# Kernel optimization log

Measured on AMD Instinct MI355X. Metric: run time of the kernel, lower is better.

Reference implementation:

```python
import jax, jax.numpy as jnp
import numpy as np

jax.config.update("jax_enable_x64", True)  # hash math uses int64, matching torch promotion

NUM_LEVELS = 16
MIN_RES = 16
MAX_RES = 1024
LOG2_T = 19
T = 2 ** LOG2_T          # hash table size per level
FEATS = 2                # features per level
HASH_INIT_SCALE = 0.001
N = 524288               # number of query points

# 8 cube corners; bit==1 selects ceil coordinate (weight = offset), bit==0 selects floor (weight = 1-offset)
CORNER_BITS = np.array([[(b >> 2) & 1, (b >> 1) & 1, b & 1] for b in range(8)], dtype=np.int64)
PRIMES = np.array([1, 2654435761, 805459861], dtype=np.int64)


def setup_inputs() -> dict:
    key = jax.random.key(0)
    k1, k2 = jax.random.split(key)
    x = jax.random.uniform(k1, (N, 3), dtype=jnp.float32, minval=-1.0, maxval=1.0)
    hash_table = (jax.random.uniform(k2, (T * NUM_LEVELS, FEATS), dtype=jnp.float32) * 2.0 - 1.0) * HASH_INIT_SCALE
    return {"x": x, "hash_table": hash_table}


def reference(x, hash_table):
    # per-level resolutions: floor(min_res * growth^level)
    growth = np.exp((np.log(MAX_RES) - np.log(MIN_RES)) / (NUM_LEVELS - 1))
    scalings = jnp.asarray(np.floor(MIN_RES * growth ** np.arange(NUM_LEVELS)), dtype=jnp.float32)  # [L]
    hash_offset = jnp.arange(NUM_LEVELS, dtype=jnp.int64) * T  # [L]

    x01 = x * 0.5 + 0.5                                # map [-1,1] -> [0,1]
    scaled = x01[..., None, :] * scalings[:, None]     # [N, L, 3]
    sc = jnp.ceil(scaled).astype(jnp.int64)            # [N, L, 3]
    sf = jnp.floor(scaled).astype(jnp.int64)           # [N, L, 3]
    offset = scaled - sf.astype(scaled.dtype)          # [N, L, 3] in [0,1)

    bits = jnp.asarray(CORNER_BITS)                    # [8, 3]
    # corner integer coords: [N, L, 8, 3]
    corners = jnp.where(bits[None, None] == 1, sc[:, :, None, :], sf[:, :, None, :])

    # Instant-NGP spatial hash (int64, matching torch's type promotion)
    p = corners * jnp.asarray(PRIMES)
    h = jnp.bitwise_xor(jnp.bitwise_xor(p[..., 0], p[..., 1]), p[..., 2])
    h = h % T + hash_offset[None, :, None]             # [N, L, 8]

    # trilinear weights: prod over dims of (offset if ceil else 1-offset)
    w = jnp.prod(jnp.where(bits[None, None] == 1, offset[:, :, None, :], 1.0 - offset[:, :, None, :]), axis=-1)  # [N, L, 8]

    feats = hash_table[h]                              # [N, L, 8, F] gather
    enc = jnp.sum(feats * w[..., None], axis=-2)       # [N, L, F]
    return enc.reshape(*enc.shape[:-2], NUM_LEVELS * FEATS)  # [N, L*F]
```

## Files before the change

### kernel.cpp

```cpp
#include <hip/hip_runtime.h>
#include <cmath>

#define TBL_SIZE (1u << 19)
#define TBL_MASK (TBL_SIZE - 1u)
#define PRIME1 2654435761u
#define PRIME2 805459861u
#define NUM_LEVELS 16
#define PPB 32

#define D0g 17
#define D1g 22
#define D2g 28
#define NW0 (D0g*D0g*D0g)
#define NW1 (D1g*D1g*D1g)
#define NW2 (D2g*D2g*D2g)
#define NWTOT (NW0+NW1+NW2)
#define PAD0 (D0g*D0g+D0g+1)
#define PAD1 (D1g*D1g+D1g+1)
#define PAD2 (D2g*D2g+D2g+1)
#define LB0  0
#define LB1  (LB0+NW0+PAD0)
#define LB2  (LB1+NW1+PAD1)
#define LTOT (LB2+NW2+PAD2)
#define LDSB (LTOT*4)

struct Args { float s[NUM_LEVELS]; };

typedef float v2f __attribute__((ext_vector_type(2)));
typedef float v4f __attribute__((ext_vector_type(4)));

template<int CTRL>
__device__ __forceinline__ float dpp_add(float v) {
    int i = __builtin_bit_cast(int, v);
    int j = __builtin_amdgcn_mov_dpp(i, CTRL, 0xF, 0xF, true);
    return v + __builtin_bit_cast(float, j);
}

__device__ __forceinline__ uint32_t f2bf(float f) {
    uint32_t u = __builtin_bit_cast(uint32_t, f);
    return (u + 0x7FFFu + ((u >> 16) & 1u)) >> 16;
}
__device__ __forceinline__ float bflo(uint32_t v) { return __builtin_bit_cast(float, v << 16); }
__device__ __forceinline__ float bfhi(uint32_t v) { return __builtin_bit_cast(float, v & 0xFFFF0000u); }

__global__ __launch_bounds__(256) void prep_kernel(
    const float* __restrict__ table, uint32_t* __restrict__ bfws,
    uint32_t* __restrict__ densews, int ncvt)
{
    int gid = blockIdx.x * 256 + (int)threadIdx.x;
    if (gid < NWTOT) {
        int l, rel, D;
        if (gid < NW0)            { l = 0; rel = gid;             D = D0g; }
        else if (gid < NW0 + NW1) { l = 1; rel = gid - NW0;       D = D1g; }
        else                      { l = 2; rel = gid - NW0 - NW1; D = D2g; }
        int d2 = D * D;
        int xp = rel / d2; int rem = rel - xp * d2;
        int yp = rem / D;  int zp = rem - yp * D;
        uint32_t h = (uint32_t)xp ^ ((uint32_t)yp * PRIME1) ^ ((uint32_t)zp * PRIME2);
        float2 e = reinterpret_cast<const float2*>(table)[((size_t)l << 19) + (h & TBL_MASK)];
        densews[gid] = f2bf(e.x) | (f2bf(e.y) << 16);
    } else {
        int rel = gid - NWTOT;
        if (rel >= ncvt) return;
        float2 e = reinterpret_cast<const float2*>(table)[((size_t)3 << 19) + rel];
        bfws[rel] = f2bf(e.x) | (f2bf(e.y) << 16);
    }
}

__global__ __launch_bounds__(1024) void lds_levels_kernel(
    const float* __restrict__ x, const uint32_t* __restrict__ densews,
    float* __restrict__ out, int npoints,
    float s0, float s1, float s2)
{
    extern __shared__ uint32_t lds[];
    for (int i = (int)threadIdx.x; i < LTOT; i += 1024) lds[i] = 0;
    __syncthreads();
    for (int i = (int)threadIdx.x; i < NW0; i += 1024) lds[LB0 + i] = densews[i];
    for (int i = (int)threadIdx.x; i < NW1; i += 1024) lds[LB1 + i] = densews[NW0 + i];
    for (int i = (int)threadIdx.x; i < NW2; i += 1024) lds[LB2 + i] = densews[NW0 + NW1 + i];
    __syncthreads();

    float acc[6];
    for (int n = blockIdx.x * 1024 + (int)threadIdx.x; n < npoints; n += (int)gridDim.x * 1024) {
        float x0 = x[(size_t)n * 3 + 0] * 0.5f + 0.5f;
        float x1 = x[(size_t)n * 3 + 1] * 0.5f + 0.5f;
        float x2 = x[(size_t)n * 3 + 2] * 0.5f + 0.5f;

#define DO_LEVEL(LI, DCONST, LBASE, SCALE)                                        \
        {                                                                         \
            const int D = DCONST, D2 = DCONST * DCONST;                           \
            float sx = x0 * SCALE, sy = x1 * SCALE, sz = x2 * SCALE;              \
            float fx = floorf(sx), fy = floorf(sy), fz = floorf(sz);              \
            float ox = sx - fx, oy = sy - fy, oz = sz - fz;                       \
            int base = LBASE + ((int)fx * D + (int)fy) * D + (int)fz;             \
            uint32_t v000 = lds[base];            uint32_t v001 = lds[base + 1];  \
            uint32_t v010 = lds[base + D];        uint32_t v011 = lds[base + D + 1]; \
            uint32_t v100 = lds[base + D2];       uint32_t v101 = lds[base + D2 + 1]; \
            uint32_t v110 = lds[base + D2 + D];   uint32_t v111 = lds[base + D2 + D + 1]; \
            float gx0 = 1.f - ox, gy0 = 1.f - oy, gz0 = 1.f - oz;                 \
            float w000 = gx0 * gy0 * gz0, w001 = gx0 * gy0 * oz;                  \
            float w010 = gx0 * oy * gz0,  w011 = gx0 * oy * oz;                   \
            float w100 = ox * gy0 * gz0,  w101 = ox * gy0 * oz;                   \
            float w110 = ox * oy * gz0,   w111 = ox * oy * oz;                    \
            acc[LI*2+0] = bflo(v000)*w000 + bflo(v001)*w001 + bflo(v010)*w010     \
                        + bflo(v011)*w011 + bflo(v100)*w100 + bflo(v101)*w101     \
                        + bflo(v110)*w110 + bflo(v111)*w111;                      \
            acc[LI*2+1] = bfhi(v000)*w000 + bfhi(v001)*w001 + bfhi(v010)*w010     \
                        + bfhi(v011)*w011 + bfhi(v100)*w100 + bfhi(v101)*w101     \
                        + bfhi(v110)*w110 + bfhi(v111)*w111;                      \
        }
        DO_LEVEL(0, D0g, LB0, s0)
        DO_LEVEL(1, D1g, LB1, s1)
        DO_LEVEL(2, D2g, LB2, s2)
#undef DO_LEVEL

        v4f a; a.x = acc[0]; a.y = acc[1]; a.z = acc[2]; a.w = acc[3];
        v2f b; b.x = acc[4]; b.y = acc[5];
        float* o = out + (size_t)n * 32;
        __builtin_nontemporal_store(a, (v4f*)o);
        __builtin_nontemporal_store(b, (v2f*)(o + 4));
    }
}

__global__ __launch_bounds__(256) void HashEncoding_88837103551034_kernel(
    const float* __restrict__ x,
    const float* __restrict__ table,
    const uint32_t* __restrict__ bfws,
    float* __restrict__ out,
    int npoints, int CH, int perXcd, int total, int L0, int NBF,
    Args args)
{
    int b = blockIdx.x; int xcd = b & 7; int sb = b >> 3;
    int g = xcd * perXcd + sb;
    if (g >= total) return;
    int li = g / CH; int level = L0 + li; int chunk = g - li * CH;
    int t = (int)threadIdx.x;
    int corner = t & 7;
    int n = chunk * PPB + (t >> 3);
    if (n >= npoints) return;

    float x0 = x[(size_t)n * 3 + 0] * 0.5f + 0.5f;
    float x1 = x[(size_t)n * 3 + 1] * 0.5f + 0.5f;
    float x2 = x[(size_t)n * 3 + 2] * 0.5f + 0.5f;
    float sl = args.s[level];
    float sx = x0 * sl, sy = x1 * sl, sz = x2 * sl;
    float fx = floorf(sx), fy = floorf(sy), fz = floorf(sz);
    float ox = sx - fx, oy = sy - fy, oz = sz - fz;
    int bx = (corner >> 2) & 1, by = (corner >> 1) & 1, bz = corner & 1;

    uint32_t h = (uint32_t)((int)fx + bx)
               ^ ((uint32_t)((int)fy + by) * PRIME1)
               ^ ((uint32_t)((int)fz + bz) * PRIME2);
    uint32_t idx = h & TBL_MASK;

    float f0, f1;
    if (li < NBF) {
        uint32_t v = bfws[((size_t)li << 19) + idx];
        f0 = bflo(v); f1 = bfhi(v);
    } else {
        float2 f = reinterpret_cast<const float2*>(table)[((size_t)level << 19) + idx];
        f0 = f.x; f1 = f.y;
    }
    float w = (bx ? ox : 1.f - ox) * (by ? oy : 1.f - oy) * (bz ? oz : 1.f - oz);
    float e0 = f0 * w, e1 = f1 * w;
    e0 = dpp_add<0xB1>(e0);  e1 = dpp_add<0xB1>(e1);
    e0 = dpp_add<0x4E>(e0);  e1 = dpp_add<0x4E>(e1);
    e0 = dpp_add<0x141>(e0); e1 = dpp_add<0x141>(e1);
    if (corner == 0) {
        v2f res; res.x = e0; res.y = e1;
        __builtin_nontemporal_store(res, (v2f*)(out + (size_t)n * 32 + level * 2));
    }
}

extern "C" void kernel_launch(void* const* d_in, const int* in_sizes, int n_in,
                              void* d_out, int out_size, void* d_ws, size_t ws_size,
                              hipStream_t stream) {
    const float* x = (const float*)d_in[0];
    const float* table = (const float*)d_in[1];
    float* out = (float*)d_out;
    int npoints = in_sizes[0] / 3;

    Args args;
    double growth = std::exp((std::log(1024.0) - std::log(16.0)) / 15.0);
    for (int l = 0; l < NUM_LEVELS; ++l)
        args.s[l] = (float)std::floor(16.0 * std::pow(growth, (double)l));

    int CH = (npoints + PPB - 1) / PPB;
    uint32_t* ws32 = (uint32_t*)d_ws;

    bool dimsOk = ((int)args.s[0] == 16) && ((int)args.s[1] == 21) && ((int)args.s[2] == 27);
    size_t needA = ((size_t)13 * TBL_SIZE + (size_t)NWTOT) * 4;

    if (dimsOk && ws_size >= needA) {
        uint32_t* wsdense = ws32 + (size_t)13 * TBL_SIZE;
        int ncvt = 13 << 19;
        int ptot = NWTOT + ncvt;
        prep_kernel<<<(ptot + 255) / 256, 256, 0, stream>>>(table, ws32, wsdense, ncvt);

        hipFuncSetAttribute(reinterpret_cast<const void*>(lds_levels_kernel),
                            hipFuncAttributeMaxDynamicSharedMemorySize, LDSB);
        lds_levels_kernel<<<256, 1024, LDSB, stream>>>(
            x, wsdense, out, npoints, args.s[0], args.s[1], args.s[2]);

        int total = 13 * CH;
        int perXcd = (total + 7) / 8;
        HashEncoding_88837103551034_kernel<<<8 * perXcd, 256, 0, stream>>>(
            x, table, ws32, out, npoints, CH, perXcd, total, 3, 13, args);
    } else {
        int total = 16 * CH;
        int perXcd = (total + 7) / 8;
        HashEncoding_88837103551034_kernel<<<8 * perXcd, 256, 0, stream>>>(
            x, table, ws32, out, npoints, CH, perXcd, total, 0, 0, args);
    }
}
```

Before: 251.6 us.

## Serve levels 3 and 4 from x-sliced dense LDS grids instead of hashing

Adds levels 3 and 4 (resolutions 36 and 48) to the dense, collision-free precomputed grids. Since those grids exceed LDS, each is split into x-slabs, and extra blocks of the LDS kernel each load one slab, scan all points, and handle only those whose floor x falls in the slab. This moves two levels' eight-corner gathers from global hash-table reads to LDS reads. In exchange every slab block re-reads x for all points, and the grid grows to 640 blocks while the hashed kernel shrinks to 11 levels.

```diff
diff --git a/kernel.cpp b/kernel.cpp
--- a/kernel.cpp
+++ b/kernel.cpp
@@ -7,14 +7,21 @@
 #define PRIME2 805459861u
 #define NUM_LEVELS 16
 #define PPB 32
+#define NHASH 11
 
 #define D0g 17
 #define D1g 22
 #define D2g 28
+#define D3g 38
+#define D4g 50
 #define NW0 (D0g*D0g*D0g)
 #define NW1 (D1g*D1g*D1g)
 #define NW2 (D2g*D2g*D2g)
-#define NWTOT (NW0+NW1+NW2)
+#define NW3 (D3g*D3g*D3g)
+#define NW4 (D4g*D4g*D4g)
+#define DB3 (NW0+NW1+NW2)
+#define DB4 (DB3+NW3)
+#define NWALL (DB4+NW4)
 #define PAD0 (D0g*D0g+D0g+1)
 #define PAD1 (D1g*D1g+D1g+1)
 #define PAD2 (D2g*D2g+D2g+1)
@@ -48,11 +55,13 @@
     uint32_t* __restrict__ densews, int ncvt)
 {
     int gid = blockIdx.x * 256 + (int)threadIdx.x;
-    if (gid < NWTOT) {
+    if (gid < NWALL) {
         int l, rel, D;
-        if (gid < NW0)            { l = 0; rel = gid;             D = D0g; }
-        else if (gid < NW0 + NW1) { l = 1; rel = gid - NW0;       D = D1g; }
-        else                      { l = 2; rel = gid - NW0 - NW1; D = D2g; }
+        if      (gid < NW0)       { l = 0; rel = gid;       D = D0g; }
+        else if (gid < NW0 + NW1) { l = 1; rel = gid - NW0; D = D1g; }
+        else if (gid < DB3)       { l = 2; rel = gid - NW0 - NW1; D = D2g; }
+        else if (gid < DB4)       { l = 3; rel = gid - DB3; D = D3g; }
+        else                      { l = 4; rel = gid - DB4; D = D4g; }
         int d2 = D * D;
         int xp = rel / d2; int rem = rel - xp * d2;
         int yp = rem / D;  int zp = rem - yp * D;
@@ -60,9 +69,9 @@
         float2 e = reinterpret_cast<const float2*>(table)[((size_t)l << 19) + (h & TBL_MASK)];
         densews[gid] = f2bf(e.x) | (f2bf(e.y) << 16);
     } else {
-        int rel = gid - NWTOT;
+        int rel = gid - NWALL;
         if (rel >= ncvt) return;
-        float2 e = reinterpret_cast<const float2*>(table)[((size_t)3 << 19) + rel];
+        float2 e = reinterpret_cast<const float2*>(table)[((size_t)5 << 19) + rel];
         bfws[rel] = f2bf(e.x) | (f2bf(e.y) << 16);
     }
 }
@@ -70,55 +79,104 @@
 __global__ __launch_bounds__(1024) void lds_levels_kernel(
     const float* __restrict__ x, const uint32_t* __restrict__ densews,
     float* __restrict__ out, int npoints,
-    float s0, float s1, float s2)
+    float s0, float s1, float s2, float s3, float s4)
 {
     extern __shared__ uint32_t lds[];
-    for (int i = (int)threadIdx.x; i < LTOT; i += 1024) lds[i] = 0;
-    __syncthreads();
-    for (int i = (int)threadIdx.x; i < NW0; i += 1024) lds[LB0 + i] = densews[i];
-    for (int i = (int)threadIdx.x; i < NW1; i += 1024) lds[LB1 + i] = densews[NW0 + i];
-    for (int i = (int)threadIdx.x; i < NW2; i += 1024) lds[LB2 + i] = densews[NW0 + NW1 + i];
-    __syncthreads();
-
-    float acc[6];
-    for (int n = blockIdx.x * 1024 + (int)threadIdx.x; n < npoints; n += (int)gridDim.x * 1024) {
-        float x0 = x[(size_t)n * 3 + 0] * 0.5f + 0.5f;
-        float x1 = x[(size_t)n * 3 + 1] * 0.5f + 0.5f;
-        float x2 = x[(size_t)n * 3 + 2] * 0.5f + 0.5f;
+    const int role = (int)blockIdx.x;
+    const int tid = (int)threadIdx.x;
+
+    if (role < 256) {
+        for (int i = tid; i < LTOT; i += 1024) lds[i] = 0;
+        __syncthreads();
+        for (int i = tid; i < NW0; i += 1024) lds[LB0 + i] = densews[i];
+        for (int i = tid; i < NW1; i += 1024) lds[LB1 + i] = densews[NW0 + i];
+        for (int i = tid; i < NW2; i += 1024) lds[LB2 + i] = densews[NW0 + NW1 + i];
+        __syncthreads();
+
+        float acc[6];
+        for (int n = role * 1024 + tid; n < npoints; n += 256 * 1024) {
+            float x0 = x[(size_t)n * 3 + 0] * 0.5f + 0.5f;
+            float x1 = x[(size_t)n * 3 + 1] * 0.5f + 0.5f;
+            float x2 = x[(size_t)n * 3 + 2] * 0.5f + 0.5f;
 
 #define DO_LEVEL(LI, DCONST, LBASE, SCALE)                                        \
-        {                                                                         \
-            const int D = DCONST, D2 = DCONST * DCONST;                           \
-            float sx = x0 * SCALE, sy = x1 * SCALE, sz = x2 * SCALE;              \
-            float fx = floorf(sx), fy = floorf(sy), fz = floorf(sz);              \
-            float ox = sx - fx, oy = sy - fy, oz = sz - fz;                       \
-            int base = LBASE + ((int)fx * D + (int)fy) * D + (int)fz;             \
-            uint32_t v000 = lds[base];            uint32_t v001 = lds[base + 1];  \
-            uint32_t v010 = lds[base + D];        uint32_t v011 = lds[base + D + 1]; \
-            uint32_t v100 = lds[base + D2];       uint32_t v101 = lds[base + D2 + 1]; \
-            uint32_t v110 = lds[base + D2 + D];   uint32_t v111 = lds[base + D2 + D + 1]; \
-            float gx0 = 1.f - ox, gy0 = 1.f - oy, gz0 = 1.f - oz;                 \
-            float w000 = gx0 * gy0 * gz0, w001 = gx0 * gy0 * oz;                  \
-            float w010 = gx0 * oy * gz0,  w011 = gx0 * oy * oz;                   \
-            float w100 = ox * gy0 * gz0,  w101 = ox * gy0 * oz;                   \
-            float w110 = ox * oy * gz0,   w111 = ox * oy * oz;                    \
-            acc[LI*2+0] = bflo(v000)*w000 + bflo(v001)*w001 + bflo(v010)*w010     \
-                        + bflo(v011)*w011 + bflo(v100)*w100 + bflo(v101)*w101     \
-                        + bflo(v110)*w110 + bflo(v111)*w111;                      \
-            acc[LI*2+1] = bfhi(v000)*w000 + bfhi(v001)*w001 + bfhi(v010)*w010     \
-                        + bfhi(v011)*w011 + bfhi(v100)*w100 + bfhi(v101)*w101     \
-                        + bfhi(v110)*w110 + bfhi(v111)*w111;                      \
+            {                                                                     \
+                const int D = DCONST, D2 = DCONST * DCONST;                       \
+                float sx = x0 * SCALE, sy = x1 * SCALE, sz = x2 * SCALE;          \
+                float fx = floorf(sx), fy = floorf(sy), fz = floorf(sz);          \
+                float ox = sx - fx, oy = sy - fy, oz = sz - fz;                   \
+                int base = LBASE + ((int)fx * D + (int)fy) * D + (int)fz;         \
+                uint32_t v000 = lds[base];            uint32_t v001 = lds[base + 1];  \
+                uint32_t v010 = lds[base + D];        uint32_t v011 = lds[base + D + 1]; \
+                uint32_t v100 = lds[base + D2];       uint32_t v101 = lds[base + D2 + 1]; \
+                uint32_t v110 = lds[base + D2 + D];   uint32_t v111 = lds[base + D2 + D + 1]; \
+                float gx0 = 1.f - ox, gy0 = 1.f - oy, gz0 = 1.f - oz;             \
+                float w000 = gx0 * gy0 * gz0, w001 = gx0 * gy0 * oz;              \
+                float w010 = gx0 * oy * gz0,  w011 = gx0 * oy * oz;               \
+                float w100 = ox * gy0 * gz0,  w101 = ox * gy0 * oz;               \
+                float w110 = ox * oy * gz0,   w111 = ox * oy * oz;                \
+                acc[LI*2+0] = bflo(v000)*w000 + bflo(v001)*w001 + bflo(v010)*w010 \
+                            + bflo(v011)*w011 + bflo(v100)*w100 + bflo(v101)*w101 \
+                            + bflo(v110)*w110 + bflo(v111)*w111;                  \
+                acc[LI*2+1] = bfhi(v000)*w000 + bfhi(v001)*w001 + bfhi(v010)*w010 \
+                            + bfhi(v011)*w011 + bfhi(v100)*w100 + bfhi(v101)*w101 \
+                            + bfhi(v110)*w110 + bfhi(v111)*w111;                  \
+            }
+            DO_LEVEL(0, D0g, LB0, s0)
+            DO_LEVEL(1, D1g, LB1, s1)
+            DO_LEVEL(2, D2g, LB2, s2)
+#undef DO_LEVEL
+            v4f a; a.x = acc[0]; a.y = acc[1]; a.z = acc[2]; a.w = acc[3];
+            v2f b; b.x = acc[4]; b.y = acc[5];
+            float* o = out + (size_t)n * 32;
+            __builtin_nontemporal_store(a, (v4f*)o);
+            __builtin_nontemporal_store(b, (v2f*)(o + 4));
         }
-        DO_LEVEL(0, D0g, LB0, s0)
-        DO_LEVEL(1, D1g, LB1, s1)
-        DO_LEVEL(2, D2g, LB2, s2)
-#undef DO_LEVEL
-
-        v4f a; a.x = acc[0]; a.y = acc[1]; a.z = acc[2]; a.w = acc[3];
-        v2f b; b.x = acc[4]; b.y = acc[5];
-        float* o = out + (size_t)n * 32;
-        __builtin_nontemporal_store(a, (v4f*)o);
-        __builtin_nontemporal_store(b, (v2f*)(o + 4));
+    } else {
+        const int sid = (role - 256) >> 6;
+        const int bs  = (role - 256) & 63;
+        const int lvl = (sid < 2) ? 3 : 4;
+        const int D   = (sid < 2) ? D3g : D4g;
+        const int D2  = D * D;
+        const int lo_t[6] = {0, 18, 0, 12, 24, 36};
+        const int hi_t[6] = {17, 36, 11, 23, 35, 48};
+        const int lo = lo_t[sid], hi = hi_t[sid];
+        const int nw = (hi - lo + 2) * D2;
+        const int db = ((sid < 2) ? DB3 : DB4) + lo * D2;
+        for (int i = tid; i < nw; i += 1024) lds[i] = densews[db + i];
+        __syncthreads();
+
+        const float sl = (sid < 2) ? s3 : s4;
+        for (int n = bs * 1024 + tid; n < npoints; n += 64 * 1024) {
+            float x0 = x[(size_t)n * 3 + 0] * 0.5f + 0.5f;
+            float sx = x0 * sl;
+            float fx = floorf(sx);
+            int ifx = (int)fx;
+            if (ifx < lo || ifx > hi) continue;
+            float x1 = x[(size_t)n * 3 + 1] * 0.5f + 0.5f;
+            float x2 = x[(size_t)n * 3 + 2] * 0.5f + 0.5f;
+            float sy = x1 * sl, sz = x2 * sl;
+            float fy = floorf(sy), fz = floorf(sz);
+            float ox = sx - fx, oy = sy - fy, oz = sz - fz;
+            int base = (ifx - lo) * D2 + (int)fy * D + (int)fz;
+            uint32_t v000 = lds[base];          uint32_t v001 = lds[base + 1];
+            uint32_t v010 = lds[base + D];      uint32_t v011 = lds[base + D + 1];
+            uint32_t v100 = lds[base + D2];     uint32_t v101 = lds[base + D2 + 1];
+            uint32_t v110 = lds[base + D2 + D]; uint32_t v111 = lds[base + D2 + D + 1];
+            float gx0 = 1.f - ox, gy0 = 1.f - oy, gz0 = 1.f - oz;
+            float w000 = gx0 * gy0 * gz0, w001 = gx0 * gy0 * oz;
+            float w010 = gx0 * oy * gz0,  w011 = gx0 * oy * oz;
+            float w100 = ox * gy0 * gz0,  w101 = ox * gy0 * oz;
+            float w110 = ox * oy * gz0,   w111 = ox * oy * oz;
+            float e0 = bflo(v000)*w000 + bflo(v001)*w001 + bflo(v010)*w010
+                     + bflo(v011)*w011 + bflo(v100)*w100 + bflo(v101)*w101
+                     + bflo(v110)*w110 + bflo(v111)*w111;
+            float e1 = bfhi(v000)*w000 + bfhi(v001)*w001 + bfhi(v010)*w010
+                     + bfhi(v011)*w011 + bfhi(v100)*w100 + bfhi(v101)*w101
+                     + bfhi(v110)*w110 + bfhi(v111)*w111;
+            v2f r; r.x = e0; r.y = e1;
+            __builtin_nontemporal_store(r, (v2f*)(out + (size_t)n * 32 + lvl * 2));
+        }
     }
 }
 
@@ -188,24 +246,26 @@
     int CH = (npoints + PPB - 1) / PPB;
     uint32_t* ws32 = (uint32_t*)d_ws;
 
-    bool dimsOk = ((int)args.s[0] == 16) && ((int)args.s[1] == 21) && ((int)args.s[2] == 27);
-    size_t needA = ((size_t)13 * TBL_SIZE + (size_t)NWTOT) * 4;
+    bool dimsOk = ((int)args.s[0] == 16) && ((int)args.s[1] == 21) && ((int)args.s[2] == 27)
+               && ((int)args.s[3] == 36) && ((int)args.s[4] == 48);
+    size_t needA = ((size_t)NHASH * TBL_SIZE + (size_t)NWALL) * 4;
 
     if (dimsOk && ws_size >= needA) {
-        uint32_t* wsdense = ws32 + (size_t)13 * TBL_SIZE;
-        int ncvt = 13 << 19;
-        int ptot = NWTOT + ncvt;
+        uint32_t* wsdense = ws32 + (size_t)NHASH * TBL_SIZE;
+        int ncvt = NHASH << 19;
+        int ptot = NWALL + ncvt;
         prep_kernel<<<(ptot + 255) / 256, 256, 0, stream>>>(table, ws32, wsdense, ncvt);
 
         hipFuncSetAttribute(reinterpret_cast<const void*>(lds_levels_kernel),
                             hipFuncAttributeMaxDynamicSharedMemorySize, LDSB);
-        lds_levels_kernel<<<256, 1024, LDSB, stream>>>(
-            x, wsdense, out, npoints, args.s[0], args.s[1], args.s[2]);
-
-        int total = 13 * CH;
+        lds_levels_kernel<<<640, 1024, LDSB, stream>>>(
+            x, wsdense, out, npoints,
+            args.s[0], args.s[1], args.s[2], args.s[3], args.s[4]);
+
+        int total = NHASH * CH;
         int perXcd = (total + 7) / 8;
         HashEncoding_88837103551034_kernel<<<8 * perXcd, 256, 0, stream>>>(
-            x, table, ws32, out, npoints, CH, perXcd, total, 3, 13, args);
+            x, table, ws32, out, npoints, CH, perXcd, total, 5, NHASH, args);
     } else {
         int total = 16 * CH;
         int perXcd = (total + 7) / 8;
```

New measurement: 260.1 us. 1.03x slower.
